# Optimization experiments

Hardware: AMD Instinct MI355X
Metric: run time of the kernel (lower is better)

The kernel has to match this reference:

```python
import jax, jax.numpy as jnp
import numpy as np

N_FINE = 50000
N_COARSE = 25000
N_EDGES = 800000
DIM = 128


def setup_inputs() -> dict:
    key = jax.random.key(0)
    k1, k2, k3, k4, k5 = jax.random.split(key, 5)
    feat = jax.random.normal(k1, (N_COARSE, DIM), dtype=jnp.float32)
    src = jax.random.randint(k2, (N_EDGES,), 0, N_FINE, dtype=jnp.int32)
    dst = jax.random.randint(k3, (N_EDGES,), 0, N_FINE, dtype=jnp.int32)
    # select_idx must be unique fine-graph ids (scatter-set semantics)
    select_idx = jax.random.permutation(k4, N_FINE)[:N_COARSE].astype(jnp.int32)
    # GraphConv params (glorot-ish init)
    weight = jax.random.normal(k5, (DIM, DIM), dtype=jnp.float32) / np.sqrt(DIM)
    bias = jnp.zeros((DIM,), dtype=jnp.float32)
    return {"feat": feat, "src": src, "dst": dst, "select_idx": select_idx,
            "weight": weight, "bias": bias, "num_nodes": N_FINE}


def reference(feat, src, dst, select_idx, weight, bias, num_nodes):
    # 1) Unpool: scatter coarse features into zero fine-graph tensor
    d = feat.shape[-1]
    fine = jnp.zeros((num_nodes, d), dtype=feat.dtype).at[select_idx].set(feat)
    # (dropout is identity in eval mode)
    # 2) GraphConv, norm='both': D_dst^{-1/2} A D_src^{-1/2} X W + b
    ones_e = jnp.ones_like(src, dtype=feat.dtype)
    deg_out = jnp.clip(jax.ops.segment_sum(ones_e, src, num_segments=num_nodes), 1.0)
    deg_in = jnp.clip(jax.ops.segment_sum(ones_e, dst, num_segments=num_nodes), 1.0)
    h = fine * (deg_out ** -0.5)[:, None]          # [N, d] source-side norm
    h = h @ weight                                  # in_feats == out_feats -> mm first
    agg = jax.ops.segment_sum(h[src], dst, num_segments=num_nodes)  # SpMM
    out = agg * (deg_in ** -0.5)[:, None] + bias
    return out
```

## Files before the change

### kernel.cpp

```cpp
#include <hip/hip_runtime.h>

#define DIM 128
#define NBC 128
#define SP 6252
#define NBKT 512

typedef __attribute__((ext_vector_type(8))) short bf16x8;
typedef __attribute__((ext_vector_type(4))) float f32x4;

static __device__ inline short f2bf(float f) {
    union { float f; unsigned u; } x;
    x.f = f;
    unsigned r = (x.u + 0x7FFF + ((x.u >> 16) & 1)) >> 16;
    return (short)r;
}
static __device__ inline float bflo(unsigned u) {
    union { unsigned u; float f; } x; x.u = u << 16; return x.f;
}
static __device__ inline float bfhi(unsigned u) {
    union { unsigned u; float f; } x; x.u = u & 0xFFFF0000u; return x.f;
}

__global__ __launch_bounds__(512) void k_hist(
    const int* __restrict__ src, const int* __restrict__ dst,
    unsigned* __restrict__ partial, int n_edges, int nhalf, int chunk) {
    __shared__ unsigned hist[SP];
    int b = blockIdx.x & (NBC - 1);
    int h = (blockIdx.x >> 7) & 1;
    int cls = blockIdx.x >> 8;
    const int* __restrict__ idx = cls ? dst : src;
    int lo = h * nhalf;

    for (int i = threadIdx.x * 4; i < SP; i += 512 * 4)
        *(uint4*)&hist[i] = make_uint4(0, 0, 0, 0);
    __syncthreads();

    int e0 = b * chunk;
    int e1 = min(e0 + chunk, n_edges);
    int qs = e0 >> 2, qe = e1 >> 2;
#define CNT(x)                                                                     \
    {                                                                              \
        unsigned t = (unsigned)((x) - lo);                                         \
        if (t < (unsigned)nhalf) atomicAdd(&hist[t >> 2], 1u << ((t & 3) * 8));    \
    }
    for (int q = qs + threadIdx.x; q < qe; q += 512) {
        int4 v = ((const int4*)idx)[q];
        CNT(v.x); CNT(v.y); CNT(v.z); CNT(v.w);
    }
    for (int e = (qe << 2) + threadIdx.x; e < e1; e += 512) CNT(idx[e]);
#undef CNT
    __syncthreads();

    unsigned* dp = partial + (size_t)((cls * 2 + h) * NBC + b) * SP;
    for (int i = threadIdx.x * 4; i < SP; i += 512 * 4)
        *(uint4*)&dp[i] = *(const uint4*)&hist[i];
}

__global__ __launch_bounds__(256) void k_hreduce(
    unsigned* __restrict__ partial, float* __restrict__ rso,
    int* __restrict__ deg, float* __restrict__ ri, int* __restrict__ map,
    int* __restrict__ off0, int* __restrict__ blksum,
    int nhalf, int nbh, int n_fine, int n_coarse) {
    int g = blockIdx.x;
    int cls = g / (2 * nbh);
    int rem = g - cls * (2 * nbh);
    int h = rem / nbh;
    int blk = rem - h * nbh;
    int hw = nhalf / 4;
    int w = blk * 256 + threadIdx.x;
    bool valid = (w < hw);

    if (cls == 0) {
        if (!valid) return;
        unsigned s = 0;
        const unsigned* p = partial + (size_t)(h * NBC) * SP + w;
#pragma unroll 8
        for (int b = 0; b < NBC; ++b) s += p[(size_t)b * SP];
        int i0 = h * nhalf + 4 * w;
        int dd[4] = {(int)(s & 255), (int)((s >> 8) & 255), (int)((s >> 16) & 255), (int)(s >> 24)};
        for (int k = 0; k < 4 && i0 + k < n_fine; ++k)
            rso[i0 + k] = rsqrtf((float)max(dd[k], 1));
        return;
    }

    __shared__ int sL[256];
    unsigned run = 0;
    if (valid) {
        unsigned* p = partial + (size_t)((2 + h) * NBC) * SP + w;
#pragma unroll 8
        for (int b = 0; b < NBC; ++b) {
            unsigned* q = p + (size_t)b * SP;
            unsigned t = *q;
            *q = run;
            run += t;
        }
    }
    int d0 = run & 255, d1 = (run >> 8) & 255, d2 = (run >> 16) & 255, d3 = run >> 24;
    int mysum = valid ? (d0 + d1 + d2 + d3) : 0;
    int t = threadIdx.x;
    sL[t] = mysum;
    __syncthreads();
    for (int dd = 1; dd < 256; dd <<= 1) {
        int x = (t >= dd) ? sL[t - dd] : 0;
        __syncthreads();
        if (t >= dd) sL[t] += x;
        __syncthreads();
    }
    int excl = sL[t] - mysum;
    if (t == 255) blksum[h * nbh + blk] = sL[255];
    if (valid) {
        int i0 = h * nhalf + 4 * w;
        int dd[4] = {d0, d1, d2, d3};
        int pf[4] = {excl, excl + d0, excl + d0 + d1, excl + d0 + d1 + d2};
        for (int k = 0; k < 4 && i0 + k < n_fine; ++k) {
            deg[i0 + k] = dd[k];
            ri[i0 + k] = rsqrtf((float)max(dd[k], 1));
            map[i0 + k] = n_coarse;
            off0[i0 + k] = pf[k];
        }
    }
}

__global__ __launch_bounds__(256) void k_prep(
    const int* __restrict__ sel, int* __restrict__ map, int* __restrict__ blksum,
    unsigned short* __restrict__ hwb, int n_coarse, int nbw) {
    int t = threadIdx.x;
    if (blockIdx.x == 0) {
        if (t < 64) {
            int orig = (t < nbw) ? blksum[t] : 0;
            int v = orig;
#pragma unroll
            for (int dd = 1; dd < 64; dd <<= 1) {
                int x = __shfl_up(v, dd, 64);
                if (t >= dd) v += x;
            }
            if (t < nbw) blksum[t] = v - orig;
        } else if (t >= 128) {
            hwb[(size_t)n_coarse * DIM + (t - 128)] = 0;
        }
    }
    int gi = blockIdx.x * 256 + t;
    if (gi < n_coarse) map[sel[gi]] = gi;
}

union SMem {
    short Wl[16384];
    unsigned cur[3200];
};

__global__ __launch_bounds__(512) void k_work(
    const int* __restrict__ src, const int* __restrict__ dst, const int* __restrict__ map,
    const int* __restrict__ off0, const int* __restrict__ blksum,
    const unsigned* __restrict__ partial, int* __restrict__ bucket,
    const float* __restrict__ feat, const int* __restrict__ sel,
    const float* __restrict__ rso, const float* __restrict__ W,
    unsigned short* __restrict__ hwb,
    int n_edges, int nhalf, int nbh, int chunk, int n_coarse) {
    __shared__ SMem sm;
    int t = threadIdx.x;

    if (blockIdx.x < NBKT) {
        int b = blockIdx.x & (NBC - 1);
        int q = blockIdx.x >> 7;
        int h = q >> 1;
        int qw = nhalf / 8;
        int qrange = nhalf / 2;
        const unsigned* pfx = partial + (size_t)((2 + h) * NBC + b) * SP + (q & 1) * qw;
        for (int i = t; i < qw; i += 512) sm.cur[i] = pfx[i];
        __syncthreads();

        int lo = q * qrange;
        int e0 = b * chunk;
        int e1 = min(e0 + chunk, n_edges);
        int qs = e0 >> 2, qe = e1 >> 2;
#define PROC(d, s)                                                                 \
    {                                                                              \
        unsigned tt = (unsigned)((d) - lo);                                        \
        if (tt < (unsigned)qrange) {                                               \
            int sh = (tt & 3) * 8;                                                 \
            unsigned old = atomicAdd(&sm.cur[tt >> 2], 1u << sh);                  \
            int widx = h * nbh + (((d) - h * nhalf) >> 10);                        \
            bucket[off0[d] + blksum[widx] + (int)((old >> sh) & 255)] = map[s];    \
        }                                                                          \
    }
        for (int qq = qs + t; qq < qe; qq += 512) {
            int4 d4 = ((const int4*)dst)[qq];
            int4 s4 = ((const int4*)src)[qq];
            PROC(d4.x, s4.x); PROC(d4.y, s4.y); PROC(d4.z, s4.z); PROC(d4.w, s4.w);
        }
        for (int e = (qe << 2) + t; e < e1; e += 512) PROC(dst[e], src[e]);
#undef PROC
        return;
    }

    int gb = blockIdx.x - NBKT;
    int ngb = gridDim.x - NBKT;
    for (int g = t; g < 2048; g += 512) {
        int n = g & 127;
        int kk = g >> 7;
        int kbase = ((kk >> 2) * 32) + ((kk & 3) * 8);
        bf16x8 v;
#pragma unroll
        for (int j = 0; j < 8; ++j) v[j] = f2bf(W[(size_t)(kbase + j) * DIM + n]);
        *(bf16x8*)&sm.Wl[g * 8] = v;
    }
    __syncthreads();

    int wv = t >> 6, lane = t & 63;
    int lg = lane >> 4;
    int lm = lane & 15;
    int ntiles = (n_coarse + 15) / 16;
    for (int tile = gb * 8 + wv; tile < ntiles; tile += ngb * 8) {
        int r0 = tile * 16;
        int ra = min(r0 + lm, n_coarse - 1);
        const float* fr = feat + (size_t)ra * DIM;
        bf16x8 a[4];
#pragma unroll
        for (int kc = 0; kc < 4; ++kc) {
            float4 x0 = *(const float4*)(fr + kc * 32 + lg * 8);
            float4 x1 = *(const float4*)(fr + kc * 32 + lg * 8 + 4);
            bf16x8 av;
            av[0] = f2bf(x0.x); av[1] = f2bf(x0.y); av[2] = f2bf(x0.z); av[3] = f2bf(x0.w);
            av[4] = f2bf(x1.x); av[5] = f2bf(x1.y); av[6] = f2bf(x1.z); av[7] = f2bf(x1.w);
            a[kc] = av;
        }
        f32x4 acc[8];
#pragma unroll
        for (int cb = 0; cb < 8; ++cb) acc[cb] = (f32x4){0.f, 0.f, 0.f, 0.f};
#pragma unroll
        for (int kc = 0; kc < 4; ++kc) {
#pragma unroll
            for (int cb = 0; cb < 8; ++cb) {
                bf16x8 b = *(const bf16x8*)&sm.Wl[(((kc * 4 + lg) * 128) + cb * 16 + lm) * 8];
                acc[cb] = __builtin_amdgcn_mfma_f32_16x16x32_bf16(a[kc], b, acc[cb], 0, 0, 0);
            }
        }
#pragma unroll
        for (int j = 0; j < 4; ++j) {
            int r = r0 + lg * 4 + j;
            if (r < n_coarse) {
                float sc = rso[sel[r]];
                unsigned short* hr = hwb + (size_t)r * DIM + lm;
#pragma unroll
                for (int cb = 0; cb < 8; ++cb)
                    hr[cb * 16] = (unsigned short)f2bf(acc[cb][j] * sc);
            }
        }
    }
}

__global__ __launch_bounds__(256) void k_gather(
    const int* __restrict__ off0, const int* __restrict__ blksum,
    const int* __restrict__ deg, const float* __restrict__ ri,
    const int* __restrict__ bucket, const uint4* __restrict__ hwb4,
    const float* __restrict__ bias, float* __restrict__ out,
    int n_fine, int nhalf, int nbh) {
    int gid = blockIdx.x * 256 + threadIdx.x;
    int l = gid & 15;
    int grp = gid >> 4;
    int ngrp = (gridDim.x * 256) >> 4;
    float4 b0 = ((const float4*)bias)[l * 2];
    float4 b1 = ((const float4*)bias)[l * 2 + 1];
    for (int v = grp; v < n_fine; v += ngrp) {
        int hh = (v >= nhalf) ? 1 : 0;
        int widx = hh * nbh + ((v - hh * nhalf) >> 10);
        int o = off0[v] + blksum[widx];
        int n = deg[v];
        float a0 = 0, a1 = 0, a2 = 0, a3 = 0, a4 = 0, a5 = 0, a6 = 0, a7 = 0;
        float c0 = 0, c1 = 0, c2 = 0, c3 = 0, c4 = 0, c5 = 0, c6 = 0, c7 = 0;
        int j = 0;
        for (; j + 4 <= n; j += 4) {
            int i0 = __builtin_nontemporal_load(bucket + o + j);
            int i1 = __builtin_nontemporal_load(bucket + o + j + 1);
            int i2 = __builtin_nontemporal_load(bucket + o + j + 2);
            int i3 = __builtin_nontemporal_load(bucket + o + j + 3);
            uint4 u0 = hwb4[(size_t)i0 * 16 + l];
            uint4 u1 = hwb4[(size_t)i1 * 16 + l];
            uint4 u2 = hwb4[(size_t)i2 * 16 + l];
            uint4 u3 = hwb4[(size_t)i3 * 16 + l];
            a0 += bflo(u0.x); a1 += bfhi(u0.x); a2 += bflo(u0.y); a3 += bfhi(u0.y);
            a4 += bflo(u0.z); a5 += bfhi(u0.z); a6 += bflo(u0.w); a7 += bfhi(u0.w);
            c0 += bflo(u1.x); c1 += bfhi(u1.x); c2 += bflo(u1.y); c3 += bfhi(u1.y);
            c4 += bflo(u1.z); c5 += bfhi(u1.z); c6 += bflo(u1.w); c7 += bfhi(u1.w);
            a0 += bflo(u2.x); a1 += bfhi(u2.x); a2 += bflo(u2.y); a3 += bfhi(u2.y);
            a4 += bflo(u2.z); a5 += bfhi(u2.z); a6 += bflo(u2.w); a7 += bfhi(u2.w);
            c0 += bflo(u3.x); c1 += bfhi(u3.x); c2 += bflo(u3.y); c3 += bfhi(u3.y);
            c4 += bflo(u3.z); c5 += bfhi(u3.z); c6 += bflo(u3.w); c7 += bfhi(u3.w);
        }
        for (; j < n; ++j) {
            int i0 = __builtin_nontemporal_load(bucket + o + j);
            uint4 u0 = hwb4[(size_t)i0 * 16 + l];
            a0 += bflo(u0.x); a1 += bfhi(u0.x); a2 += bflo(u0.y); a3 += bfhi(u0.y);
            a4 += bflo(u0.z); a5 += bfhi(u0.z); a6 += bflo(u0.w); a7 += bfhi(u0.w);
        }
        float s = ri[v];
        f32x4 r0, r1;
        r0.x = (a0 + c0) * s + b0.x; r0.y = (a1 + c1) * s + b0.y;
        r0.z = (a2 + c2) * s + b0.z; r0.w = (a3 + c3) * s + b0.w;
        r1.x = (a4 + c4) * s + b1.x; r1.y = (a5 + c5) * s + b1.y;
        r1.z = (a6 + c6) * s + b1.z; r1.w = (a7 + c7) * s + b1.w;
        __builtin_nontemporal_store(r0, (f32x4*)(out + (size_t)v * DIM + l * 8));
        __builtin_nontemporal_store(r1, (f32x4*)(out + (size_t)v * DIM + l * 8 + 4));
    }
}

extern "C" void kernel_launch(void* const* d_in, const int* in_sizes, int n_in,
                              void* d_out, int out_size, void* d_ws, size_t ws_size,
                              hipStream_t stream) {
    const float* feat = (const float*)d_in[0];
    const int* src = (const int*)d_in[1];
    const int* dst = (const int*)d_in[2];
    const int* sel = (const int*)d_in[3];
    const float* W = (const float*)d_in[4];
    const float* bias = (const float*)d_in[5];
    float* out = (float*)d_out;

    int n_fine = out_size / DIM;
    int n_coarse = in_sizes[0] / DIM;
    int n_edges = in_sizes[1];

    int nhalf = ((n_fine / 2) + 3) & ~3;
    int nbh = (nhalf / 4 + 255) / 256;
    int nbw = 2 * nbh;
    int chunk = ((n_edges + NBC - 1) / NBC + 3) & ~3;

    int* map = (int*)d_ws;
    int* off0 = map + n_fine;
    int* deg = off0 + n_fine;
    float* ri = (float*)(deg + n_fine);
    float* rso = ri + n_fine;
    int* blksum = (int*)(rso + n_fine);
    unsigned short* hwb = (unsigned short*)(blksum + 64);
    int* bucket = (int*)(hwb + (size_t)(n_coarse + 1) * DIM);
    unsigned* partial = (unsigned*)(bucket + n_edges);

    int ntiles = (n_coarse + 15) / 16;
    int ngb = (ntiles + 7) / 8;

    hipLaunchKernelGGL(k_hist, dim3(4 * NBC), dim3(512), 0, stream,
                       src, dst, partial, n_edges, nhalf, chunk);
    hipLaunchKernelGGL(k_hreduce, dim3(4 * nbh), dim3(256), 0, stream,
                       partial, rso, deg, ri, map, off0, blksum, nhalf, nbh, n_fine, n_coarse);
    hipLaunchKernelGGL(k_prep, dim3((n_coarse + 255) / 256), dim3(256), 0, stream,
                       sel, map, blksum, hwb, n_coarse, nbw);
    hipLaunchKernelGGL(k_work, dim3(NBKT + ngb), dim3(512), 0, stream,
                       src, dst, map, off0, blksum, partial, bucket,
                       feat, sel, rso, W, hwb, n_edges, nhalf, nbh, chunk, n_coarse);
    hipLaunchKernelGGL(k_gather, dim3((n_fine * 16 + 255) / 256), dim3(256), 0, stream,
                       off0, blksum, deg, ri, bucket, (const uint4*)hwb, bias, out,
                       n_fine, nhalf, nbh);
}
```

Measured before the change: 80.89 us.

## Drop edges from unselected sources from CSR buckets and gather

Builds the coarse-to-fine map before the histogram pass so the dst histogram can count only edges whose source is a selected coarse node. Buckets and the gather loop then cover only these active edges, which should cut bucket writes and gather reads roughly in half. The in-degree normalisation still uses the full count. Window sizes are hard-coded to the problem dimensions, and two small map-init kernels are added. The block-sum scan moves into the consumer kernels, and the dummy zero row is no longer written.

```diff
diff --git a/kernel.cpp b/kernel.cpp
--- a/kernel.cpp
+++ b/kernel.cpp
@@ -2,8 +2,12 @@
 
 #define DIM 128
 #define NBC 128
-#define SP 6252
+#define QS 13312
+#define QW 3328
+#define HS 26624
+#define HW 6656
 #define NBKT 512
+#define NWIN 52
 
 typedef __attribute__((ext_vector_type(8))) short bf16x8;
 typedef __attribute__((ext_vector_type(4))) float f32x4;
@@ -21,83 +25,120 @@
     union { unsigned u; float f; } x; x.u = u & 0xFFFF0000u; return x.f;
 }
 
+__global__ void k_m0(int* __restrict__ map, int n_fine, int n_coarse) {
+    int i = blockIdx.x * 256 + threadIdx.x;
+    if (i < n_fine) map[i] = n_coarse;
+}
+__global__ void k_m1(const int* __restrict__ sel, int* __restrict__ map, int n_sel) {
+    int i = blockIdx.x * 256 + threadIdx.x;
+    if (i < n_sel) map[sel[i]] = i;
+}
+
 __global__ __launch_bounds__(512) void k_hist(
-    const int* __restrict__ src, const int* __restrict__ dst,
-    unsigned* __restrict__ partial, int n_edges, int nhalf, int chunk) {
-    __shared__ unsigned hist[SP];
-    int b = blockIdx.x & (NBC - 1);
-    int h = (blockIdx.x >> 7) & 1;
-    int cls = blockIdx.x >> 8;
-    const int* __restrict__ idx = cls ? dst : src;
-    int lo = h * nhalf;
-
-    for (int i = threadIdx.x * 4; i < SP; i += 512 * 4)
-        *(uint4*)&hist[i] = make_uint4(0, 0, 0, 0);
+    const int* __restrict__ src, const int* __restrict__ dst, const int* __restrict__ map,
+    unsigned* __restrict__ p_src, unsigned* __restrict__ p_tot, unsigned* __restrict__ p_act,
+    int n_edges, int n_coarse, int chunk) {
+    __shared__ unsigned sm[HW];
+    int t = threadIdx.x;
+
+    for (int i = t * 4; i < HW; i += 512 * 4)
+        *(uint4*)&sm[i] = make_uint4(0, 0, 0, 0);
     __syncthreads();
 
-    int e0 = b * chunk;
-    int e1 = min(e0 + chunk, n_edges);
-    int qs = e0 >> 2, qe = e1 >> 2;
-#define CNT(x)                                                                     \
-    {                                                                              \
-        unsigned t = (unsigned)((x) - lo);                                         \
-        if (t < (unsigned)nhalf) atomicAdd(&hist[t >> 2], 1u << ((t & 3) * 8));    \
-    }
-    for (int q = qs + threadIdx.x; q < qe; q += 512) {
-        int4 v = ((const int4*)idx)[q];
-        CNT(v.x); CNT(v.y); CNT(v.z); CNT(v.w);
-    }
-    for (int e = (qe << 2) + threadIdx.x; e < e1; e += 512) CNT(idx[e]);
+    if (blockIdx.x < 256) {
+        int h = blockIdx.x >> 7;
+        int b = blockIdx.x & (NBC - 1);
+        int lo = h * HS;
+        int e0 = b * chunk, e1 = min(e0 + chunk, n_edges);
+        int qs = e0 >> 2, qe = e1 >> 2;
+#define CNT(x)                                                                  \
+    {                                                                           \
+        unsigned tt = (unsigned)((x) - lo);                                     \
+        if (tt < (unsigned)HS) atomicAdd(&sm[tt >> 2], 1u << ((tt & 3) * 8));   \
+    }
+        for (int q = qs + t; q < qe; q += 512) {
+            int4 v = ((const int4*)src)[q];
+            CNT(v.x); CNT(v.y); CNT(v.z); CNT(v.w);
+        }
+        for (int e = (qe << 2) + t; e < e1; e += 512) CNT(src[e]);
 #undef CNT
-    __syncthreads();
-
-    unsigned* dp = partial + (size_t)((cls * 2 + h) * NBC + b) * SP;
-    for (int i = threadIdx.x * 4; i < SP; i += 512 * 4)
-        *(uint4*)&dp[i] = *(const uint4*)&hist[i];
+        __syncthreads();
+        unsigned* dp = p_src + (size_t)(h * NBC + b) * HW;
+        for (int i = t * 4; i < HW; i += 512 * 4)
+            *(uint4*)&dp[i] = *(const uint4*)&sm[i];
+    } else {
+        int idx2 = blockIdx.x - 256;
+        int q = idx2 >> 7;
+        int b = idx2 & (NBC - 1);
+        int lo = q * QS;
+        int e0 = b * chunk, e1 = min(e0 + chunk, n_edges);
+        int qs = e0 >> 2, qe = e1 >> 2;
+#define PROC(d, s)                                                              \
+    {                                                                           \
+        unsigned tt = (unsigned)((d) - lo);                                     \
+        if (tt < (unsigned)QS) {                                                \
+            unsigned inc = 1u << ((tt & 3) * 8);                                \
+            atomicAdd(&sm[tt >> 2], inc);                                       \
+            if (map[s] != n_coarse) atomicAdd(&sm[QW + (tt >> 2)], inc);        \
+        }                                                                       \
+    }
+        for (int qq = qs + t; qq < qe; qq += 512) {
+            int4 d4 = ((const int4*)dst)[qq];
+            int4 s4 = ((const int4*)src)[qq];
+            PROC(d4.x, s4.x); PROC(d4.y, s4.y); PROC(d4.z, s4.z); PROC(d4.w, s4.w);
+        }
+        for (int e = (qe << 2) + t; e < e1; e += 512) PROC(dst[e], src[e]);
+#undef PROC
+        __syncthreads();
+        unsigned* dpt = p_tot + (size_t)(q * NBC + b) * QW;
+        unsigned* dpa = p_act + (size_t)(q * NBC + b) * QW;
+        for (int i = t * 4; i < QW; i += 512 * 4) {
+            *(uint4*)&dpt[i] = *(const uint4*)&sm[i];
+            *(uint4*)&dpa[i] = *(const uint4*)&sm[QW + i];
+        }
+    }
 }
 
 __global__ __launch_bounds__(256) void k_hreduce(
-    unsigned* __restrict__ partial, float* __restrict__ rso,
-    int* __restrict__ deg, float* __restrict__ ri, int* __restrict__ map,
-    int* __restrict__ off0, int* __restrict__ blksum,
-    int nhalf, int nbh, int n_fine, int n_coarse) {
-    int g = blockIdx.x;
-    int cls = g / (2 * nbh);
-    int rem = g - cls * (2 * nbh);
-    int h = rem / nbh;
-    int blk = rem - h * nbh;
-    int hw = nhalf / 4;
-    int w = blk * 256 + threadIdx.x;
-    bool valid = (w < hw);
-
-    if (cls == 0) {
-        if (!valid) return;
+    const unsigned* __restrict__ p_src, const unsigned* __restrict__ p_tot,
+    unsigned* __restrict__ p_act, float* __restrict__ rso,
+    int* __restrict__ deg_act, float* __restrict__ ri,
+    int* __restrict__ off0, int* __restrict__ blksum, int n_fine) {
+    int t = threadIdx.x;
+
+    if (blockIdx.x < 52) {
+        int h = blockIdx.x / 26;
+        int blk = blockIdx.x - h * 26;
+        int w = blk * 256 + t;
         unsigned s = 0;
-        const unsigned* p = partial + (size_t)(h * NBC) * SP + w;
+        const unsigned* p = p_src + (size_t)(h * NBC) * HW + w;
 #pragma unroll 8
-        for (int b = 0; b < NBC; ++b) s += p[(size_t)b * SP];
-        int i0 = h * nhalf + 4 * w;
+        for (int b = 0; b < NBC; ++b) s += p[(size_t)b * HW];
+        int i0 = h * HS + 4 * w;
         int dd[4] = {(int)(s & 255), (int)((s >> 8) & 255), (int)((s >> 16) & 255), (int)(s >> 24)};
         for (int k = 0; k < 4 && i0 + k < n_fine; ++k)
             rso[i0 + k] = rsqrtf((float)max(dd[k], 1));
         return;
     }
 
+    int idx2 = blockIdx.x - 52;
+    int q = idx2 / 13;
+    int blk = idx2 - q * 13;
+    int w = blk * 256 + t;
+    const unsigned* pt = p_tot + (size_t)(q * NBC) * QW + w;
+    unsigned* pa = p_act + (size_t)(q * NBC) * QW + w;
+    unsigned s_tot = 0, run = 0;
+#pragma unroll 8
+    for (int b = 0; b < NBC; ++b) {
+        s_tot += pt[(size_t)b * QW];
+        unsigned v = pa[(size_t)b * QW];
+        pa[(size_t)b * QW] = run;
+        run += v;
+    }
+    int a0 = run & 255, a1 = (run >> 8) & 255, a2 = (run >> 16) & 255, a3 = run >> 24;
+    int mysum = a0 + a1 + a2 + a3;
+
     __shared__ int sL[256];
-    unsigned run = 0;
-    if (valid) {
-        unsigned* p = partial + (size_t)((2 + h) * NBC) * SP + w;
-#pragma unroll 8
-        for (int b = 0; b < NBC; ++b) {
-            unsigned* q = p + (size_t)b * SP;
-            unsigned t = *q;
-            *q = run;
-            run += t;
-        }
-    }
-    int d0 = run & 255, d1 = (run >> 8) & 255, d2 = (run >> 16) & 255, d3 = run >> 24;
-    int mysum = valid ? (d0 + d1 + d2 + d3) : 0;
-    int t = threadIdx.x;
     sL[t] = mysum;
     __syncthreads();
     for (int dd = 1; dd < 256; dd <<= 1) {
@@ -107,81 +148,69 @@
         __syncthreads();
     }
     int excl = sL[t] - mysum;
-    if (t == 255) blksum[h * nbh + blk] = sL[255];
-    if (valid) {
-        int i0 = h * nhalf + 4 * w;
-        int dd[4] = {d0, d1, d2, d3};
-        int pf[4] = {excl, excl + d0, excl + d0 + d1, excl + d0 + d1 + d2};
-        for (int k = 0; k < 4 && i0 + k < n_fine; ++k) {
-            deg[i0 + k] = dd[k];
-            ri[i0 + k] = rsqrtf((float)max(dd[k], 1));
-            map[i0 + k] = n_coarse;
-            off0[i0 + k] = pf[k];
-        }
-    }
-}
-
-__global__ __launch_bounds__(256) void k_prep(
-    const int* __restrict__ sel, int* __restrict__ map, int* __restrict__ blksum,
-    unsigned short* __restrict__ hwb, int n_coarse, int nbw) {
+    int win = q * 13 + blk;
+    if (t == 255) blksum[win] = sL[255];
+
+    int i0 = q * QS + 4 * w;
+    int aa[4] = {a0, a1, a2, a3};
+    int tt[4] = {(int)(s_tot & 255), (int)((s_tot >> 8) & 255),
+                 (int)((s_tot >> 16) & 255), (int)(s_tot >> 24)};
+    int pf[4] = {excl, excl + a0, excl + a0 + a1, excl + a0 + a1 + a2};
+    for (int k = 0; k < 4 && i0 + k < n_fine; ++k) {
+        deg_act[i0 + k] = aa[k];
+        ri[i0 + k] = rsqrtf((float)max(tt[k], 1));
+        off0[i0 + k] = pf[k];
+    }
+}
+
+union SMem {
+    short Wl[16384];
+    struct { unsigned cur[QW]; int bscan[64]; } bk;
+};
+
+__global__ __launch_bounds__(512) void k_work(
+    const int* __restrict__ src, const int* __restrict__ dst, const int* __restrict__ map,
+    const int* __restrict__ off0, const int* __restrict__ blksum,
+    const unsigned* __restrict__ p_act, int* __restrict__ bucket,
+    const float* __restrict__ feat, const int* __restrict__ sel,
+    const float* __restrict__ rso, const float* __restrict__ W,
+    unsigned short* __restrict__ hwb,
+    int n_edges, int chunk, int n_coarse) {
+    __shared__ SMem sm;
     int t = threadIdx.x;
-    if (blockIdx.x == 0) {
+
+    if (blockIdx.x < NBKT) {
+        int q = blockIdx.x >> 7;
+        int b = blockIdx.x & (NBC - 1);
+        const unsigned* pfx = p_act + (size_t)(q * NBC + b) * QW;
+        for (int i = t; i < QW; i += 512) sm.bk.cur[i] = pfx[i];
         if (t < 64) {
-            int orig = (t < nbw) ? blksum[t] : 0;
-            int v = orig;
+            int v = (t < NWIN) ? blksum[t] : 0;
+            int orig = v;
 #pragma unroll
             for (int dd = 1; dd < 64; dd <<= 1) {
                 int x = __shfl_up(v, dd, 64);
                 if (t >= dd) v += x;
             }
-            if (t < nbw) blksum[t] = v - orig;
-        } else if (t >= 128) {
-            hwb[(size_t)n_coarse * DIM + (t - 128)] = 0;
-        }
-    }
-    int gi = blockIdx.x * 256 + t;
-    if (gi < n_coarse) map[sel[gi]] = gi;
-}
-
-union SMem {
-    short Wl[16384];
-    unsigned cur[3200];
-};
-
-__global__ __launch_bounds__(512) void k_work(
-    const int* __restrict__ src, const int* __restrict__ dst, const int* __restrict__ map,
-    const int* __restrict__ off0, const int* __restrict__ blksum,
-    const unsigned* __restrict__ partial, int* __restrict__ bucket,
-    const float* __restrict__ feat, const int* __restrict__ sel,
-    const float* __restrict__ rso, const float* __restrict__ W,
-    unsigned short* __restrict__ hwb,
-    int n_edges, int nhalf, int nbh, int chunk, int n_coarse) {
-    __shared__ SMem sm;
-    int t = threadIdx.x;
-
-    if (blockIdx.x < NBKT) {
-        int b = blockIdx.x & (NBC - 1);
-        int q = blockIdx.x >> 7;
-        int h = q >> 1;
-        int qw = nhalf / 8;
-        int qrange = nhalf / 2;
-        const unsigned* pfx = partial + (size_t)((2 + h) * NBC + b) * SP + (q & 1) * qw;
-        for (int i = t; i < qw; i += 512) sm.cur[i] = pfx[i];
-        __syncthreads();
-
-        int lo = q * qrange;
-        int e0 = b * chunk;
-        int e1 = min(e0 + chunk, n_edges);
+            sm.bk.bscan[t] = v - orig;
+        }
+        __syncthreads();
+
+        int lo = q * QS;
+        int e0 = b * chunk, e1 = min(e0 + chunk, n_edges);
         int qs = e0 >> 2, qe = e1 >> 2;
-#define PROC(d, s)                                                                 \
-    {                                                                              \
-        unsigned tt = (unsigned)((d) - lo);                                        \
-        if (tt < (unsigned)qrange) {                                               \
-            int sh = (tt & 3) * 8;                                                 \
-            unsigned old = atomicAdd(&sm.cur[tt >> 2], 1u << sh);                  \
-            int widx = h * nbh + (((d) - h * nhalf) >> 10);                        \
-            bucket[off0[d] + blksum[widx] + (int)((old >> sh) & 255)] = map[s];    \
-        }                                                                          \
+#define PROC(d, s)                                                                  \
+    {                                                                               \
+        unsigned tt = (unsigned)((d) - lo);                                         \
+        if (tt < (unsigned)QS) {                                                    \
+            int c = map[s];                                                         \
+            if (c != n_coarse) {                                                    \
+                int sh = (tt & 3) * 8;                                              \
+                unsigned old = atomicAdd(&sm.bk.cur[tt >> 2], 1u << sh);            \
+                bucket[off0[d] + sm.bk.bscan[(d) >> 10] + (int)((old >> sh) & 255)] \
+                    = c;                                                            \
+            }                                                                       \
+        }                                                                           \
     }
         for (int qq = qs + t; qq < qe; qq += 512) {
             int4 d4 = ((const int4*)dst)[qq];
@@ -251,21 +280,32 @@
 
 __global__ __launch_bounds__(256) void k_gather(
     const int* __restrict__ off0, const int* __restrict__ blksum,
-    const int* __restrict__ deg, const float* __restrict__ ri,
+    const int* __restrict__ deg_act, const float* __restrict__ ri,
     const int* __restrict__ bucket, const uint4* __restrict__ hwb4,
-    const float* __restrict__ bias, float* __restrict__ out,
-    int n_fine, int nhalf, int nbh) {
-    int gid = blockIdx.x * 256 + threadIdx.x;
+    const float* __restrict__ bias, float* __restrict__ out, int n_fine) {
+    __shared__ int bscan[64];
+    int t = threadIdx.x;
+    if (t < 64) {
+        int v = (t < NWIN) ? blksum[t] : 0;
+        int orig = v;
+#pragma unroll
+        for (int dd = 1; dd < 64; dd <<= 1) {
+            int x = __shfl_up(v, dd, 64);
+            if (t >= dd) v += x;
+        }
+        bscan[t] = v - orig;
+    }
+    __syncthreads();
+
+    int gid = blockIdx.x * 256 + t;
     int l = gid & 15;
     int grp = gid >> 4;
     int ngrp = (gridDim.x * 256) >> 4;
     float4 b0 = ((const float4*)bias)[l * 2];
     float4 b1 = ((const float4*)bias)[l * 2 + 1];
     for (int v = grp; v < n_fine; v += ngrp) {
-        int hh = (v >= nhalf) ? 1 : 0;
-        int widx = hh * nbh + ((v - hh * nhalf) >> 10);
-        int o = off0[v] + blksum[widx];
-        int n = deg[v];
+        int o = off0[v] + bscan[v >> 10];
+        int n = deg_act[v];
         float a0 = 0, a1 = 0, a2 = 0, a3 = 0, a4 = 0, a5 = 0, a6 = 0, a7 = 0;
         float c0 = 0, c1 = 0, c2 = 0, c3 = 0, c4 = 0, c5 = 0, c6 = 0, c7 = 0;
         int j = 0;
@@ -319,34 +359,34 @@
     int n_coarse = in_sizes[0] / DIM;
     int n_edges = in_sizes[1];
 
-    int nhalf = ((n_fine / 2) + 3) & ~3;
-    int nbh = (nhalf / 4 + 255) / 256;
-    int nbw = 2 * nbh;
     int chunk = ((n_edges + NBC - 1) / NBC + 3) & ~3;
 
     int* map = (int*)d_ws;
     int* off0 = map + n_fine;
-    int* deg = off0 + n_fine;
-    float* ri = (float*)(deg + n_fine);
+    int* deg_act = off0 + n_fine;
+    float* ri = (float*)(deg_act + n_fine);
     float* rso = ri + n_fine;
     int* blksum = (int*)(rso + n_fine);
     unsigned short* hwb = (unsigned short*)(blksum + 64);
-    int* bucket = (int*)(hwb + (size_t)(n_coarse + 1) * DIM);
-    unsigned* partial = (unsigned*)(bucket + n_edges);
+    int* bucket = (int*)(hwb + (size_t)n_coarse * DIM);
+    unsigned* p_src = (unsigned*)(bucket + n_edges);
+    unsigned* p_tot = p_src + (size_t)2 * NBC * HW;
+    unsigned* p_act = p_tot + (size_t)4 * NBC * QW;
 
     int ntiles = (n_coarse + 15) / 16;
     int ngb = (ntiles + 7) / 8;
 
-    hipLaunchKernelGGL(k_hist, dim3(4 * NBC), dim3(512), 0, stream,
-                       src, dst, partial, n_edges, nhalf, chunk);
-    hipLaunchKernelGGL(k_hreduce, dim3(4 * nbh), dim3(256), 0, stream,
-                       partial, rso, deg, ri, map, off0, blksum, nhalf, nbh, n_fine, n_coarse);
-    hipLaunchKernelGGL(k_prep, dim3((n_coarse + 255) / 256), dim3(256), 0, stream,
-                       sel, map, blksum, hwb, n_coarse, nbw);
+    hipLaunchKernelGGL(k_m0, dim3((n_fine + 255) / 256), dim3(256), 0, stream,
+                       map, n_fine, n_coarse);
+    hipLaunchKernelGGL(k_m1, dim3((n_coarse + 255) / 256), dim3(256), 0, stream,
+                       sel, map, n_coarse);
+    hipLaunchKernelGGL(k_hist, dim3(768), dim3(512), 0, stream,
+                       src, dst, map, p_src, p_tot, p_act, n_edges, n_coarse, chunk);
+    hipLaunchKernelGGL(k_hreduce, dim3(104), dim3(256), 0, stream,
+                       p_src, p_tot, p_act, rso, deg_act, ri, off0, blksum, n_fine);
     hipLaunchKernelGGL(k_work, dim3(NBKT + ngb), dim3(512), 0, stream,
-                       src, dst, map, off0, blksum, partial, bucket,
-                       feat, sel, rso, W, hwb, n_edges, nhalf, nbh, chunk, n_coarse);
+                       src, dst, map, off0, blksum, p_act, bucket,
+                       feat, sel, rso, W, hwb, n_edges, chunk, n_coarse);
     hipLaunchKernelGGL(k_gather, dim3((n_fine * 16 + 255) / 256), dim3(256), 0, stream,
-                       off0, blksum, deg, ri, bucket, (const uint4*)hwb, bias, out,
-                       n_fine, nhalf, nbh);
-}
+                       off0, blksum, deg_act, ri, bucket, (const uint4*)hwb, bias, out, n_fine);
+}
```

Result: slower. 87.60 us (+8.3%).
